# Kernel optimization log

Hardware: AMD Instinct MI355X
Metric: run time of the kernel (lower is better)

## Reference

```python
import jax, jax.numpy as jnp
import numpy as np
import math

EMB = 128
HW = 128

def setup_inputs() -> dict:
    key = jax.random.key(0)
    k_t, k1, k2, k3, k4 = jax.random.split(key, 5)
    B = 8192
    t = jax.random.uniform(k_t, (B,), dtype=jnp.float32)
    s = 1.0 / math.sqrt(EMB)
    W1 = jax.random.uniform(k1, (EMB, EMB), dtype=jnp.float32, minval=-s, maxval=s)
    b1 = jax.random.uniform(k2, (EMB,), dtype=jnp.float32, minval=-s, maxval=s)
    W2 = jax.random.uniform(k3, (EMB, EMB), dtype=jnp.float32, minval=-s, maxval=s)
    b2 = jax.random.uniform(k4, (EMB,), dtype=jnp.float32, minval=-s, maxval=s)
    return {"t": t, "W1": W1, "b1": b1, "W2": W2, "b2": b2}

def reference(t, W1, b1, W2, b2):
    # sinusoidal embedding: 64 log-spaced freqs in [1, 1000]
    freqs = jnp.exp(jnp.linspace(math.log(1.0), math.log(1000.0), EMB // 2)).astype(jnp.float32)
    ang = (2.0 * math.pi) * freqs  # [64]
    phase = t[:, None] * ang[None, :]  # [B, 64]
    emb = jnp.concatenate([jnp.sin(phase), jnp.cos(phase)], axis=-1)  # [B, 128]
    # MLP: Linear -> SiLU -> Linear -> SiLU (torch Linear: x @ W.T + b)
    h = jax.nn.silu(emb @ W1.T + b1)
    h = jax.nn.silu(h @ W2.T + b2)
    # [B,1,1,128] nearest-upsampled to [B,1,128,128]: broadcast along H
    out = jnp.broadcast_to(h[:, None, None, :], (h.shape[0], 1, HW, HW))
    return out
```

## Files before the change

### kernel.cpp

```cpp
#include <hip/hip_runtime.h>
#include <math.h>

typedef float f32x4 __attribute__((ext_vector_type(4)));

__global__ __launch_bounds__(256) void k_fused(
    const float* __restrict__ t,
    const float* __restrict__ W1, const float* __restrict__ b1,
    const float* __restrict__ W2, const float* __restrict__ b2,
    float* __restrict__ out)
{
    __shared__ float WL[128 * 128];
    __shared__ __attribute__((aligned(16))) float emb[8][128];
    __shared__ __attribute__((aligned(16))) float h1[8][128];
    __shared__ __attribute__((aligned(16))) float h2[8][128];

    const int tid  = threadIdx.x;
    const int base = blockIdx.x * 8;
    const int jj   = tid & 127;
    const int half = tid >> 7;

    {
        const f32x4* g = (const f32x4*)W1;
        #pragma unroll
        for (int it = 0; it < 16; ++it) {
            int idx4 = it * 256 + tid;
            f32x4 q = g[idx4];
            int j  = idx4 >> 5;
            int k0 = (idx4 & 31) * 4;
            #pragma unroll
            for (int i = 0; i < 4; ++i) {
                int k = k0 + i;
                WL[k * 128 + (j ^ (k & 31))] = q[i];
            }
        }
    }
    #pragma unroll
    for (int i = 0; i < 2; ++i) {
        int idx = i * 256 + tid;
        int b = idx >> 6, k = idx & 63;
        double a   = (double)k * (6.907755278982137 / 63.0);
        float freq = (float)exp(a);
        float ang  = 6.2831853071795865f * freq;
        float ph   = t[base + b] * ang;
        float sv, cv;
        sincosf(ph, &sv, &cv);
        emb[b][k]      = sv;
        emb[b][64 + k] = cv;
    }
    __syncthreads();

    {
        float acc[4];
        float bv = b1[jj];
        #pragma unroll
        for (int m = 0; m < 4; ++m) acc[m] = bv;
        #pragma unroll
        for (int k4 = 0; k4 < 32; ++k4) {
            const int k0 = k4 * 4;
            float w0 = WL[(k0 + 0) * 128 + (jj ^ ((k0 + 0) & 31))];
            float w1 = WL[(k0 + 1) * 128 + (jj ^ ((k0 + 1) & 31))];
            float w2 = WL[(k0 + 2) * 128 + (jj ^ ((k0 + 2) & 31))];
            float w3 = WL[(k0 + 3) * 128 + (jj ^ ((k0 + 3) & 31))];
            #pragma unroll
            for (int m = 0; m < 4; ++m) {
                float4 ev = ((const float4*)emb[half * 4 + m])[k4];
                acc[m] = fmaf(w0, ev.x, acc[m]);
                acc[m] = fmaf(w1, ev.y, acc[m]);
                acc[m] = fmaf(w2, ev.z, acc[m]);
                acc[m] = fmaf(w3, ev.w, acc[m]);
            }
        }
        #pragma unroll
        for (int m = 0; m < 4; ++m) {
            float a = acc[m];
            h1[half * 4 + m][jj] = a / (1.0f + expf(-a));
        }
    }
    __syncthreads();

    {
        const f32x4* g = (const f32x4*)W2;
        #pragma unroll
        for (int it = 0; it < 16; ++it) {
            int idx4 = it * 256 + tid;
            f32x4 q = g[idx4];
            int j  = idx4 >> 5;
            int k0 = (idx4 & 31) * 4;
            #pragma unroll
            for (int i = 0; i < 4; ++i) {
                int k = k0 + i;
                WL[k * 128 + (j ^ (k & 31))] = q[i];
            }
        }
    }
    __syncthreads();

    {
        float acc[4];
        float bv = b2[jj];
        #pragma unroll
        for (int m = 0; m < 4; ++m) acc[m] = bv;
        #pragma unroll
        for (int k4 = 0; k4 < 32; ++k4) {
            const int k0 = k4 * 4;
            float w0 = WL[(k0 + 0) * 128 + (jj ^ ((k0 + 0) & 31))];
            float w1 = WL[(k0 + 1) * 128 + (jj ^ ((k0 + 1) & 31))];
            float w2 = WL[(k0 + 2) * 128 + (jj ^ ((k0 + 2) & 31))];
            float w3 = WL[(k0 + 3) * 128 + (jj ^ ((k0 + 3) & 31))];
            #pragma unroll
            for (int m = 0; m < 4; ++m) {
                float4 ev = ((const float4*)h1[half * 4 + m])[k4];
                acc[m] = fmaf(w0, ev.x, acc[m]);
                acc[m] = fmaf(w1, ev.y, acc[m]);
                acc[m] = fmaf(w2, ev.z, acc[m]);
                acc[m] = fmaf(w3, ev.w, acc[m]);
            }
        }
        #pragma unroll
        for (int m = 0; m < 4; ++m) {
            float a = acc[m];
            h2[half * 4 + m][jj] = a / (1.0f + expf(-a));
        }
    }
    __syncthreads();

    #pragma unroll
    for (int m = 0; m < 8; ++m) {
        f32x4 v = *(const f32x4*)&h2[m][(tid & 31) * 4];
        f32x4* d = (f32x4*)(out + (size_t)(base + m) * 16384);
        #pragma unroll
        for (int c = 0; c < 16; ++c) {
            d[c * 256 + tid] = v;
        }
    }
}

extern "C" void kernel_launch(void* const* d_in, const int* in_sizes, int n_in,
                              void* d_out, int out_size, void* d_ws, size_t ws_size,
                              hipStream_t stream) {
    const float* t  = (const float*)d_in[0];
    const float* W1 = (const float*)d_in[1];
    const float* b1 = (const float*)d_in[2];
    const float* W2 = (const float*)d_in[3];
    const float* b2 = (const float*)d_in[4];
    float* out = (float*)d_out;
    const int B = in_sizes[0];

    k_fused<<<B / 8, 256, 0, stream>>>(t, W1, b1, W2, b2, out);
}
```

Baseline: 543.2 us.

## Process 16 rows per block with float4 swizzled weight layout

Each block now handles 16 batch rows instead of 8, which halves the number of blocks and so halves the repeated global reads and shared-memory staging of W1 and W2. Weights are stored row-major as float4 with an XOR swizzle, so each thread computes two output columns for four rows using vector LDS loads. Shared buffers are reused (EH holds the embedding and then h2) to keep LDS usage bounded. The kernel is dominated by the 512MB output write, so any gain depends on the staging overhead that remains; fewer blocks may also hurt latency hiding of the stores.

```diff
diff --git a/kernel.cpp b/kernel.cpp
--- a/kernel.cpp
+++ b/kernel.cpp
@@ -9,33 +9,30 @@
     const float* __restrict__ W2, const float* __restrict__ b2,
     float* __restrict__ out)
 {
-    __shared__ float WL[128 * 128];
-    __shared__ __attribute__((aligned(16))) float emb[8][128];
-    __shared__ __attribute__((aligned(16))) float h1[8][128];
-    __shared__ __attribute__((aligned(16))) float h2[8][128];
+    __shared__ __attribute__((aligned(16))) float4 WQ[4096];
+    __shared__ __attribute__((aligned(16))) float  EH[16 * 128];
+    __shared__ __attribute__((aligned(16))) float  H1[16 * 128];
 
     const int tid  = threadIdx.x;
-    const int base = blockIdx.x * 8;
-    const int jj   = tid & 127;
-    const int half = tid >> 7;
+    const int base = blockIdx.x * 16;
+
+    const int r0 = tid & 63;
+    const int r1 = r0 + 64;
+    const int g  = tid >> 6;
+    const int xr = tid & 31;
 
     {
-        const f32x4* g = (const f32x4*)W1;
+        const float4* gp = (const float4*)W1;
         #pragma unroll
         for (int it = 0; it < 16; ++it) {
             int idx4 = it * 256 + tid;
-            f32x4 q = g[idx4];
-            int j  = idx4 >> 5;
-            int k0 = (idx4 & 31) * 4;
-            #pragma unroll
-            for (int i = 0; i < 4; ++i) {
-                int k = k0 + i;
-                WL[k * 128 + (j ^ (k & 31))] = q[i];
-            }
+            float4 q = gp[idx4];
+            int r = idx4 >> 5, c = idx4 & 31;
+            WQ[r * 32 + (c ^ (r & 31))] = q;
         }
     }
     #pragma unroll
-    for (int i = 0; i < 2; ++i) {
+    for (int i = 0; i < 4; ++i) {
         int idx = i * 256 + tid;
         int b = idx >> 6, k = idx & 63;
         double a   = (double)k * (6.907755278982137 / 63.0);
@@ -44,89 +41,88 @@
         float ph   = t[base + b] * ang;
         float sv, cv;
         sincosf(ph, &sv, &cv);
-        emb[b][k]      = sv;
-        emb[b][64 + k] = cv;
+        EH[b * 128 + k]      = sv;
+        EH[b * 128 + 64 + k] = cv;
     }
     __syncthreads();
 
     {
-        float acc[4];
-        float bv = b1[jj];
+        float acc0[4], acc1[4];
+        float bv0 = b1[r0], bv1 = b1[r1];
         #pragma unroll
-        for (int m = 0; m < 4; ++m) acc[m] = bv;
+        for (int m = 0; m < 4; ++m) { acc0[m] = bv0; acc1[m] = bv1; }
         #pragma unroll
         for (int k4 = 0; k4 < 32; ++k4) {
-            const int k0 = k4 * 4;
-            float w0 = WL[(k0 + 0) * 128 + (jj ^ ((k0 + 0) & 31))];
-            float w1 = WL[(k0 + 1) * 128 + (jj ^ ((k0 + 1) & 31))];
-            float w2 = WL[(k0 + 2) * 128 + (jj ^ ((k0 + 2) & 31))];
-            float w3 = WL[(k0 + 3) * 128 + (jj ^ ((k0 + 3) & 31))];
+            float4 w0 = WQ[r0 * 32 + (k4 ^ xr)];
+            float4 w1 = WQ[r1 * 32 + (k4 ^ xr)];
             #pragma unroll
             for (int m = 0; m < 4; ++m) {
-                float4 ev = ((const float4*)emb[half * 4 + m])[k4];
-                acc[m] = fmaf(w0, ev.x, acc[m]);
-                acc[m] = fmaf(w1, ev.y, acc[m]);
-                acc[m] = fmaf(w2, ev.z, acc[m]);
-                acc[m] = fmaf(w3, ev.w, acc[m]);
+                float4 ev = ((const float4*)(EH + (g * 4 + m) * 128))[k4];
+                acc0[m] = fmaf(w0.x, ev.x, acc0[m]);
+                acc0[m] = fmaf(w0.y, ev.y, acc0[m]);
+                acc0[m] = fmaf(w0.z, ev.z, acc0[m]);
+                acc0[m] = fmaf(w0.w, ev.w, acc0[m]);
+                acc1[m] = fmaf(w1.x, ev.x, acc1[m]);
+                acc1[m] = fmaf(w1.y, ev.y, acc1[m]);
+                acc1[m] = fmaf(w1.z, ev.z, acc1[m]);
+                acc1[m] = fmaf(w1.w, ev.w, acc1[m]);
             }
         }
         #pragma unroll
         for (int m = 0; m < 4; ++m) {
-            float a = acc[m];
-            h1[half * 4 + m][jj] = a / (1.0f + expf(-a));
+            float a0 = acc0[m], a1 = acc1[m];
+            H1[(g * 4 + m) * 128 + r0] = a0 / (1.0f + expf(-a0));
+            H1[(g * 4 + m) * 128 + r1] = a1 / (1.0f + expf(-a1));
         }
     }
     __syncthreads();
 
     {
-        const f32x4* g = (const f32x4*)W2;
+        const float4* gp = (const float4*)W2;
         #pragma unroll
         for (int it = 0; it < 16; ++it) {
             int idx4 = it * 256 + tid;
-            f32x4 q = g[idx4];
-            int j  = idx4 >> 5;
-            int k0 = (idx4 & 31) * 4;
-            #pragma unroll
-            for (int i = 0; i < 4; ++i) {
-                int k = k0 + i;
-                WL[k * 128 + (j ^ (k & 31))] = q[i];
-            }
+            float4 q = gp[idx4];
+            int r = idx4 >> 5, c = idx4 & 31;
+            WQ[r * 32 + (c ^ (r & 31))] = q;
         }
     }
     __syncthreads();
 
     {
-        float acc[4];
-        float bv = b2[jj];
+        float acc0[4], acc1[4];
+        float bv0 = b2[r0], bv1 = b2[r1];
         #pragma unroll
-        for (int m = 0; m < 4; ++m) acc[m] = bv;
+        for (int m = 0; m < 4; ++m) { acc0[m] = bv0; acc1[m] = bv1; }
         #pragma unroll
         for (int k4 = 0; k4 < 32; ++k4) {
-            const int k0 = k4 * 4;
-            float w0 = WL[(k0 + 0) * 128 + (jj ^ ((k0 + 0) & 31))];
-            float w1 = WL[(k0 + 1) * 128 + (jj ^ ((k0 + 1) & 31))];
-            float w2 = WL[(k0 + 2) * 128 + (jj ^ ((k0 + 2) & 31))];
-            float w3 = WL[(k0 + 3) * 128 + (jj ^ ((k0 + 3) & 31))];
+            float4 w0 = WQ[r0 * 32 + (k4 ^ xr)];
+            float4 w1 = WQ[r1 * 32 + (k4 ^ xr)];
             #pragma unroll
             for (int m = 0; m < 4; ++m) {
-                float4 ev = ((const float4*)h1[half * 4 + m])[k4];
-                acc[m] = fmaf(w0, ev.x, acc[m]);
-                acc[m] = fmaf(w1, ev.y, acc[m]);
-                acc[m] = fmaf(w2, ev.z, acc[m]);
-                acc[m] = fmaf(w3, ev.w, acc[m]);
+                float4 ev = ((const float4*)(H1 + (g * 4 + m) * 128))[k4];
+                acc0[m] = fmaf(w0.x, ev.x, acc0[m]);
+                acc0[m] = fmaf(w0.y, ev.y, acc0[m]);
+                acc0[m] = fmaf(w0.z, ev.z, acc0[m]);
+                acc0[m] = fmaf(w0.w, ev.w, acc0[m]);
+                acc1[m] = fmaf(w1.x, ev.x, acc1[m]);
+                acc1[m] = fmaf(w1.y, ev.y, acc1[m]);
+                acc1[m] = fmaf(w1.z, ev.z, acc1[m]);
+                acc1[m] = fmaf(w1.w, ev.w, acc1[m]);
             }
         }
         #pragma unroll
         for (int m = 0; m < 4; ++m) {
-            float a = acc[m];
-            h2[half * 4 + m][jj] = a / (1.0f + expf(-a));
+            float a0 = acc0[m], a1 = acc1[m];
+            EH[(g * 4 + m) * 128 + r0] = a0 / (1.0f + expf(-a0));
+            EH[(g * 4 + m) * 128 + r1] = a1 / (1.0f + expf(-a1));
         }
     }
     __syncthreads();
 
     #pragma unroll
-    for (int m = 0; m < 8; ++m) {
-        f32x4 v = *(const f32x4*)&h2[m][(tid & 31) * 4];
+    for (int m = 0; m < 16; ++m) {
+        f32x4 v = *(const f32x4*)&EH[m * 128 + (tid & 31) * 4];
         f32x4* d = (f32x4*)(out + (size_t)(base + m) * 16384);
         #pragma unroll
         for (int c = 0; c < 16; ++c) {
@@ -146,5 +142,5 @@
     float* out = (float*)d_out;
     const int B = in_sizes[0];
 
-    k_fused<<<B / 8, 256, 0, stream>>>(t, W1, b1, W2, b2, out);
+    k_fused<<<B / 16, 256, 0, stream>>>(t, W1, b1, W2, b2, out);
 }
```

Measured after the change: 536.4 us. About the same (-1.2%).
